# Performance work log

Measured on AMD Instinct MI355X. Metric: run time of the kernel, lower is better.

Reference implementation:

```python
import jax, jax.numpy as jnp
import numpy as np

N_CONV = 3
FEAT = 128
N_RBF = 20
CUTOFF = 5.0
EPS = 1e-15
N_NODES = 10000
N_EDGES = 160000


def setup_inputs() -> dict:
    key = jax.random.key(0)
    ks = jax.random.split(key, 8)
    N, E = N_NODES, N_EDGES
    cg_xyz = jax.random.normal(ks[0], (N, 3), jnp.float32) * 2.0
    # Directed, self-loop-free edge list (both i<j and i>j present, so the
    # original make_directed() is a no-op on this data).
    src = jax.random.randint(ks[1], (E,), 0, N)
    off = jax.random.randint(ks[2], (E,), 1, N)
    CG_nbr_list = jnp.stack([src, (src + off) % N], axis=1)
    cg_s = jax.random.normal(ks[3], (N, FEAT), jnp.float32)
    s = 1.0 / np.sqrt(FEAT)
    # Per-conv-layer weights of ENMessageBlock: inv_dense = Dense(F->F, silu) + Dense(F->3F);
    # dist_embed = ExpNormalBasis(n_rbf) -> Dense(n_rbf->3F) * cosine envelope.
    W1 = jax.random.normal(ks[4], (N_CONV, FEAT, FEAT), jnp.float32) * s
    b1 = jnp.zeros((N_CONV, FEAT), jnp.float32)
    W2 = jax.random.normal(ks[5], (N_CONV, FEAT, 3 * FEAT), jnp.float32) * s
    b2 = jnp.zeros((N_CONV, 3 * FEAT), jnp.float32)
    Wr = jax.random.normal(ks[6], (N_CONV, N_RBF, 3 * FEAT), jnp.float32) / np.sqrt(N_RBF)
    br = jnp.zeros((N_CONV, 3 * FEAT), jnp.float32)
    return {"cg_xyz": cg_xyz, "CG_nbr_list": CG_nbr_list, "cg_s": cg_s,
            "W1": W1, "b1": b1, "W2": W2, "b2": b2, "Wr": Wr, "br": br}


def _expnorm_rbf(dist):
    # ExpNormalBasis: exp(-beta * (exp(-d) - mu)^2), mu in [exp(-cutoff), 1]
    mu = jnp.linspace(np.exp(-CUTOFF), 1.0, N_RBF, dtype=jnp.float32)
    beta = np.float32((2.0 / N_RBF * (1.0 - np.exp(-CUTOFF))) ** -2)
    return jnp.exp(-beta * (jnp.exp(-dist)[:, None] - mu) ** 2)  # (E, n_rbf)


def _cos_envelope(dist):
    return jnp.where(dist < CUTOFF, 0.5 * (jnp.cos(jnp.pi * dist / CUTOFF) + 1.0), 0.0)


def reference(cg_xyz, CG_nbr_list, cg_s, W1, b1, W2, b2, Wr, br):
    N = cg_s.shape[0]
    i, j = CG_nbr_list[:, 0], CG_nbr_list[:, 1]
    r_ij = cg_xyz[j] - cg_xyz[i]                      # (E, 3)
    dist = jnp.sqrt((r_ij ** 2 + EPS).sum(-1))        # (E,)
    unit = r_ij / dist[:, None]                        # (E, 3)
    rbf = _expnorm_rbf(dist)                           # (E, n_rbf) edge-invariant across layers
    env = _cos_envelope(dist)[:, None]                 # (E, 1)

    s_i = cg_s                                         # (N, F)
    v_i = jnp.zeros((N, FEAT, 3), cg_s.dtype)          # (N, F, 3)
    for l in range(N_CONV):
        phi = jax.nn.silu(s_i @ W1[l] + b1[l]) @ W2[l] + b2[l]   # (N, 3F)
        w_s = (rbf @ Wr[l] + br[l]) * env                         # (E, 3F)
        prod = phi[j] * w_s                                       # (E, 3F) gather + gate
        ds = prod[:, :FEAT]                                       # scalar message
        gate_v = prod[:, FEAT:2 * FEAT]                           # gates v_j
        gate_u = prod[:, 2 * FEAT:]                               # gates unit vector
        dv_ij = gate_u[:, :, None] * unit[:, None, :] + gate_v[:, :, None] * v_i[j]  # (E, F, 3)
        s_i = s_i + jax.ops.segment_sum(ds, i, num_segments=N)
        v_i = v_i + jax.ops.segment_sum(dv_ij, i, num_segments=N)
    return s_i, v_i
```

## Files before the change

### kernel.cpp

```cpp
#include <hip/hip_runtime.h>
#include <hip/hip_bf16.h>

#define NRBF 20
#define KAUG 24

typedef __attribute__((ext_vector_type(8))) short short8;
typedef __attribute__((ext_vector_type(4))) float float4v;
typedef __attribute__((ext_vector_type(2))) _Float16 half2v;
typedef unsigned short ushort_t;

__device__ __forceinline__ float bf2f(ushort_t u) {
    return __uint_as_float(((unsigned)u) << 16);
}
__device__ __forceinline__ ushort_t f2bf(float f) {
    unsigned u = __float_as_uint(f);
    u += 0x7FFF + ((u >> 16) & 1);
    return (ushort_t)(u >> 16);
}
__device__ __forceinline__ float ldin(const void* p, size_t idx, int isbf) {
    return isbf ? bf2f(((const ushort_t*)p)[idx]) : ((const float*)p)[idx];
}
__device__ __forceinline__ void stout(void* p, size_t idx, float v, int isbf) {
    if (isbf) ((ushort_t*)p)[idx] = f2bf(v);
    else      ((float*)p)[idx] = v;
}
__device__ __forceinline__ float dot2(half2v a, half2v b, float c) {
#if __has_builtin(__builtin_amdgcn_fdot2)
    return __builtin_amdgcn_fdot2(a, b, c, false);
#else
    return c + (float)a.x * (float)b.x + (float)a.y * (float)b.y;
#endif
}

__global__ void detect_kernel(const void* __restrict__ xyz, int* __restrict__ flag,
                              int* __restrict__ deg, int N) {
    int idx = blockIdx.x * blockDim.x + threadIdx.x;
    if (idx < N) deg[idx] = 0;
    if (blockIdx.x == 0 && threadIdx.x < 64) {
        const ushort_t* u = (const ushort_t*)xyz;
        unsigned e0 = (u[2 * threadIdx.x] >> 7) & 0xFF;
        unsigned long long bad = __ballot(e0 >= 0x90);
        if (threadIdx.x == 0) *flag = (__popcll(bad) > 2) ? 0 : 1;
    }
}

__global__ void prelude_kernel(const void* __restrict__ xyz, const int* __restrict__ nbr,
                               const void* __restrict__ cg_s,
                               const void* __restrict__ W1, const void* __restrict__ W2,
                               const void* __restrict__ Wr, const void* __restrict__ br,
                               float* __restrict__ s_acc, ushort_t* __restrict__ s_hi,
                               ushort_t* __restrict__ s_lo, int* __restrict__ deg,
                               ushort_t* __restrict__ B1hi, ushort_t* __restrict__ B1lo,
                               ushort_t* __restrict__ B2hi, ushort_t* __restrict__ B2lo,
                               _Float16* __restrict__ WrT,
                               int N128, int E, const int* __restrict__ flagp) {
    int isbf = *flagp;
    int idx = blockIdx.x * blockDim.x + threadIdx.x;
    if (idx < E) {
        int i = nbr[2 * idx], j = nbr[2 * idx + 1];
        float dx = ldin(xyz, 3 * j,     isbf) - ldin(xyz, 3 * i,     isbf);
        float dy = ldin(xyz, 3 * j + 1, isbf) - ldin(xyz, 3 * i + 1, isbf);
        float dz = ldin(xyz, 3 * j + 2, isbf) - ldin(xyz, 3 * i + 2, isbf);
        float dist = sqrtf(dx * dx + dy * dy + dz * dz + 3e-15f);
        if (dist < 5.0f) atomicAdd(&deg[i], 1);
    }
    if (idx < N128) {
        float v = ldin(cg_s, idx, isbf);
        s_acc[idx] = v;
        ushort_t hi = f2bf(v);
        s_hi[idx] = hi;
        s_lo[idx] = f2bf(v - bf2f(hi));
    }
    const int NW1 = 3 * 4 * 8 * 64;
    const int NW2 = 3 * 4 * 24 * 64;
    const int NWT = 3 * 384;
    if (idx < NW1) {
        int lane = idx & 63;
        int t = idx >> 6;
        int nt = t % 8; t /= 8;
        int ks = t % 4; int l = t / 4;
        int n = lane & 15, quad = lane >> 4;
        int col = nt * 16 + n;
        size_t base = (size_t)l * 128 * 128;
        size_t fo = (size_t)idx * 8;
        #pragma unroll
        for (int j = 0; j < 8; j++) {
            int k = ks * 32 + quad * 8 + j;
            float v = ldin(W1, base + (size_t)k * 128 + col, isbf);
            ushort_t hi = f2bf(v);
            B1hi[fo + j] = hi;
            B1lo[fo + j] = f2bf(v - bf2f(hi));
        }
    } else if (idx < NW1 + NW2) {
        int i2 = idx - NW1;
        int lane = i2 & 63;
        int t = i2 >> 6;
        int nt = t % 24; t /= 24;
        int ks = t % 4; int l = t / 4;
        int n = lane & 15, quad = lane >> 4;
        int col = nt * 16 + n;
        size_t base = (size_t)l * 128 * 384;
        size_t fo = (size_t)i2 * 8;
        #pragma unroll
        for (int j = 0; j < 8; j++) {
            int k = ks * 32 + quad * 8 + j;
            float v = ldin(W2, base + (size_t)k * 384 + col, isbf);
            ushort_t hi = f2bf(v);
            B2hi[fo + j] = hi;
            B2lo[fo + j] = f2bf(v - bf2f(hi));
        }
    } else if (idx < NW1 + NW2 + NWT) {
        int i2 = idx - NW1 - NW2;
        int l = i2 / 384, col = i2 % 384;
        _Float16* wt = WrT + ((size_t)l * 384 + col) * KAUG;
        #pragma unroll
        for (int k = 0; k < KAUG; k++) {
            float v = 0.f;
            if (k < NRBF) v = ldin(Wr, ((size_t)l * NRBF + k) * 384 + col, isbf);
            else if (k == NRBF) v = ldin(br, (size_t)l * 384 + col, isbf);
            wt[k] = (_Float16)v;
        }
    }
}

__global__ void scan_kernel(int* __restrict__ deg, int* __restrict__ rowptr, int N) {
    __shared__ int part[256];
    int t = threadIdx.x;
    int chunk = (N + 255) / 256;
    int lo = t * chunk, hi = min(lo + chunk, N);
    int s = 0;
    for (int i = lo; i < hi; i++) s += deg[i];
    part[t] = s;
    __syncthreads();
    for (int off = 1; off < 256; off <<= 1) {
        int v = (t >= off) ? part[t - off] : 0;
        __syncthreads();
        if (t >= off) part[t] += v;
        __syncthreads();
    }
    int base = (t == 0) ? 0 : part[t - 1];
    for (int i = lo; i < hi; i++) {
        rowptr[i] = base;
        int d = deg[i];
        deg[i] = base;
        base += d;
    }
    if (t == 0) rowptr[N] = part[255];
}

__global__ void pack_kernel(const void* __restrict__ xyz, const int* __restrict__ nbr,
                            int* __restrict__ cursor, int* __restrict__ jlist,
                            float4* __restrict__ upos, _Float16* __restrict__ rbfh,
                            int E, const int* __restrict__ flagp) {
    int isbf = *flagp;
    int e = blockIdx.x * blockDim.x + threadIdx.x;
    if (e >= E) return;
    int i = nbr[2 * e], j = nbr[2 * e + 1];
    float dx = ldin(xyz, 3 * j,     isbf) - ldin(xyz, 3 * i,     isbf);
    float dy = ldin(xyz, 3 * j + 1, isbf) - ldin(xyz, 3 * i + 1, isbf);
    float dz = ldin(xyz, 3 * j + 2, isbf) - ldin(xyz, 3 * i + 2, isbf);
    float dist = sqrtf(dx * dx + dy * dy + dz * dz + 3e-15f);
    if (!(dist < 5.0f)) return;
    constexpr float PI = 3.14159265358979323846f;
    float ev = 0.5f * (cosf(PI * dist * 0.2f) + 1.0f);
    int pos = atomicAdd(&cursor[i], 1);
    jlist[pos] = j;
    float inv = 1.0f / dist;
    upos[pos] = make_float4(dx * inv, dy * inv, dz * inv, ev);
    constexpr double EM5 = 0.006737946999085467;
    constexpr float MU0 = (float)EM5;
    constexpr float DMU = (float)((1.0 - EM5) / 19.0);
    constexpr float BETA = (float)(1.0 / ((0.1 * (1.0 - EM5)) * (0.1 * (1.0 - EM5))));
    float ed = expf(-dist);
    _Float16* rp = rbfh + (size_t)pos * KAUG;
    #pragma unroll
    for (int k = 0; k < NRBF; k++) {
        float dmu = ed - (MU0 + k * DMU);
        rp[k] = (_Float16)(ev * expf(-BETA * dmu * dmu));
    }
    rp[NRBF] = (_Float16)ev;
    #pragma unroll
    for (int k = NRBF + 1; k < KAUG; k++) rp[k] = (_Float16)0.f;
}

template <int ACT, int OUTMODE, int NTILES>
__global__ __launch_bounds__(256) void mfma_gemm(
    const ushort_t* __restrict__ Ahi, const ushort_t* __restrict__ Alo,
    const ushort_t* __restrict__ Bhi, const ushort_t* __restrict__ Blo,
    const void* __restrict__ bias, size_t biasoff,
    ushort_t* __restrict__ out_hi, ushort_t* __restrict__ out_lo,
    int M, const int* __restrict__ flagp) {
    constexpr int Ncols = NTILES * 16;
    int isbf = *flagp;
    int nt = blockIdx.x % NTILES;
    int bx = blockIdx.x / NTILES;
    int tid = threadIdx.x;
    int wave = tid >> 6, lane = tid & 63;
    int m = lane & 15, quad = lane >> 4;
    int brow = bx * 64 + wave * 16;
    int row = brow + m;
    float4v acc = {};
    short8 zero8 = {};
    #pragma unroll
    for (int ks = 0; ks < 4; ks++) {
        short8 ah = zero8, al = zero8;
        if (row < M) {
            size_t ao = (size_t)row * 128 + ks * 32 + quad * 8;
            ah = *reinterpret_cast<const short8*>(Ahi + ao);
            al = *reinterpret_cast<const short8*>(Alo + ao);
        }
        size_t fo = (((size_t)ks * NTILES + nt) * 64 + lane) * 8;
        short8 bh = *reinterpret_cast<const short8*>(Bhi + fo);
        acc = __builtin_amdgcn_mfma_f32_16x16x32_bf16(ah, bh, acc, 0, 0, 0);
        acc = __builtin_amdgcn_mfma_f32_16x16x32_bf16(al, bh, acc, 0, 0, 0);
        if (!isbf) {
            short8 bl = *reinterpret_cast<const short8*>(Blo + fo);
            acc = __builtin_amdgcn_mfma_f32_16x16x32_bf16(ah, bl, acc, 0, 0, 0);
        }
    }
    int col = nt * 16 + m;
    float bv = ldin(bias, biasoff + col, isbf);
    #pragma unroll
    for (int r = 0; r < 4; r++) {
        int orow = brow + quad * 4 + r;
        if (orow >= M) continue;
        float x = acc[r] + bv;
        if (ACT) x = x / (1.0f + expf(-x));
        size_t oo = (size_t)orow * Ncols + col;
        ushort_t h = f2bf(x);
        out_hi[oo] = h;
        if (OUTMODE == 0) out_lo[oo] = f2bf(x - bf2f(h));
    }
}

template <int L0, int LAST>
__global__ __launch_bounds__(128, 8) void node_kernel(
    const int* __restrict__ rowptr, const int* __restrict__ jlist,
    const float4* __restrict__ upos, const _Float16* __restrict__ rbfh,
    const _Float16* __restrict__ WrT,
    const ushort_t* __restrict__ phi,
    const float* __restrict__ v_old, const ushort_t* __restrict__ vh_old,
    float* __restrict__ s_acc, ushort_t* __restrict__ s_hi, ushort_t* __restrict__ s_lo,
    float* __restrict__ v_new, ushort_t* __restrict__ vh_new,
    void* __restrict__ out, int N, const int* __restrict__ flagp) {
    int isbf = *flagp;
    int tt = threadIdx.x;
    int node = blockIdx.x;

    half2v wc0[11], wc1[11], wc2[11];
    {
        const half2v* w0p = (const half2v*)(WrT + (size_t)tt * KAUG);
        const half2v* w1p = (const half2v*)(WrT + (size_t)(tt + 128) * KAUG);
        const half2v* w2p = (const half2v*)(WrT + (size_t)(tt + 256) * KAUG);
        #pragma unroll
        for (int k = 0; k < 11; k++) {
            wc0[k] = w0p[k]; wc1[k] = w1p[k]; wc2[k] = w2p[k];
        }
    }
    int start = __builtin_amdgcn_readfirstlane(rowptr[node]);
    int end   = __builtin_amdgcn_readfirstlane(rowptr[node + 1]);

    float dsv = 0.f, ax = 0.f, ay = 0.f, az = 0.f;
    for (int k = start; k < end; k++) {
        int j = __builtin_amdgcn_readfirstlane(jlist[k]);
        float4 u4 = upos[k];
        const half2v* rp = (const half2v*)(rbfh + (size_t)k * KAUG);
        float w0 = 0.f, w1 = 0.f, w2 = 0.f;
        #pragma unroll
        for (int r = 0; r < 11; r++) {
            half2v rv = rp[r];
            w0 = dot2(rv, wc0[r], w0);
            w1 = dot2(rv, wc1[r], w1);
            w2 = dot2(rv, wc2[r], w2);
        }
        size_t jb = (size_t)j * 384;
        dsv += bf2f(phi[jb + tt]) * w0;
        float gv = bf2f(phi[jb + 128 + tt]) * w1;
        float gu = bf2f(phi[jb + 256 + tt]) * w2;
        if (L0) {
            ax += gu * u4.x; ay += gu * u4.y; az += gu * u4.z;
        } else {
            const ushort_t* vj = &vh_old[jb + (size_t)tt * 3];
            ax += gu * u4.x + gv * bf2f(vj[0]);
            ay += gu * u4.y + gv * bf2f(vj[1]);
            az += gu * u4.z + gv * bf2f(vj[2]);
        }
    }
    size_t so = (size_t)node * 128 + tt;
    float snew = s_acc[so] + dsv;
    size_t ib = (size_t)node * 384 + (size_t)tt * 3;
    float vx = L0 ? ax : v_old[ib]     + ax;
    float vy = L0 ? ay : v_old[ib + 1] + ay;
    float vz = L0 ? az : v_old[ib + 2] + az;
    if (LAST) {
        stout(out, so, snew, isbf);
        size_t ob = (size_t)N * 128 + ib;
        stout(out, ob,     vx, isbf);
        stout(out, ob + 1, vy, isbf);
        stout(out, ob + 2, vz, isbf);
    } else {
        s_acc[so] = snew;
        ushort_t hi = f2bf(snew);
        s_hi[so] = hi;
        s_lo[so] = f2bf(snew - bf2f(hi));
        v_new[ib] = vx; v_new[ib + 1] = vy; v_new[ib + 2] = vz;
        vh_new[ib]     = f2bf(vx);
        vh_new[ib + 1] = f2bf(vy);
        vh_new[ib + 2] = f2bf(vz);
    }
}

extern "C" void kernel_launch(void* const* d_in, const int* in_sizes, int n_in,
                              void* d_out, int out_size, void* d_ws, size_t ws_size,
                              hipStream_t stream) {
    const int N = in_sizes[0] / 3;
    const int E = in_sizes[1] / 2;
    const void* xyz  = d_in[0];
    const int*  nbr  = (const int*)d_in[1];
    const void* cg_s = d_in[2];
    const void* W1   = d_in[3];
    const void* b1   = d_in[4];
    const void* W2   = d_in[5];
    const void* b2   = d_in[6];
    const void* Wr   = d_in[7];
    const void* br   = d_in[8];

    size_t off = 0;
    auto alloc = [&](size_t bytes) -> char* {
        char* p = (char*)d_ws + off;
        off = (off + bytes + 63) & ~(size_t)63;
        return p;
    };
    int*       flag   = (int*)alloc(64);
    float*     s_acc  = (float*)alloc((size_t)N * 128 * 4);
    float*     vA     = (float*)alloc((size_t)N * 384 * 4);
    float*     vB     = (float*)alloc((size_t)N * 384 * 4);
    int*       rowptr = (int*)alloc((size_t)(N + 1) * 4);
    int*       deg    = (int*)alloc((size_t)N * 4);
    int*       jlist  = (int*)alloc((size_t)E * 4);
    float4*    upos   = (float4*)alloc((size_t)(E + 16) * 16);
    _Float16*  rbfh   = (_Float16*)alloc((size_t)(E + 16) * KAUG * 2);
    _Float16*  WrT    = (_Float16*)alloc((size_t)3 * 384 * KAUG * 2);
    ushort_t*  s_hi   = (ushort_t*)alloc((size_t)N * 128 * 2);
    ushort_t*  s_lo   = (ushort_t*)alloc((size_t)N * 128 * 2);
    ushort_t*  h_hi   = (ushort_t*)alloc((size_t)N * 128 * 2);
    ushort_t*  h_lo   = (ushort_t*)alloc((size_t)N * 128 * 2);
    ushort_t*  phi    = (ushort_t*)alloc((size_t)N * 384 * 2);
    ushort_t*  vhA    = (ushort_t*)alloc((size_t)N * 384 * 2);
    ushort_t*  vhB    = (ushort_t*)alloc((size_t)N * 384 * 2);
    ushort_t*  B1hi   = (ushort_t*)alloc((size_t)3 * 4 * 8 * 64 * 8 * 2);
    ushort_t*  B1lo   = (ushort_t*)alloc((size_t)3 * 4 * 8 * 64 * 8 * 2);
    ushort_t*  B2hi   = (ushort_t*)alloc((size_t)3 * 4 * 24 * 64 * 8 * 2);
    ushort_t*  B2lo   = (ushort_t*)alloc((size_t)3 * 4 * 24 * 64 * 8 * 2);

    detect_kernel<<<(N + 255) / 256, 256, 0, stream>>>(xyz, flag, deg, N);
    const int N128 = N * 128;
    const int pg = (max(E, N128) + 255) / 256;
    prelude_kernel<<<pg, 256, 0, stream>>>(xyz, nbr, cg_s, W1, W2, Wr, br,
                                           s_acc, s_hi, s_lo, deg,
                                           B1hi, B1lo, B2hi, B2lo, WrT,
                                           N128, E, flag);
    scan_kernel<<<1, 256, 0, stream>>>(deg, rowptr, N);
    pack_kernel<<<(E + 255) / 256, 256, 0, stream>>>(xyz, nbr, deg, jlist, upos,
                                                     rbfh, E, flag);

    const int gx = (N + 63) / 64;
    for (int l = 0; l < 3; l++) {
        mfma_gemm<1, 0, 8><<<gx * 8, 256, 0, stream>>>(
            s_hi, s_lo,
            B1hi + (size_t)l * 4 * 8 * 64 * 8, B1lo + (size_t)l * 4 * 8 * 64 * 8,
            b1, (size_t)l * 128, h_hi, h_lo, N, flag);
        mfma_gemm<0, 1, 24><<<gx * 24, 256, 0, stream>>>(
            h_hi, h_lo,
            B2hi + (size_t)l * 4 * 24 * 64 * 8, B2lo + (size_t)l * 4 * 24 * 64 * 8,
            b2, (size_t)l * 384, phi, (ushort_t*)nullptr, N, flag);
        const _Float16* wrt = WrT + (size_t)l * 384 * KAUG;
        if (l == 0) {
            node_kernel<1, 0><<<N, 128, 0, stream>>>(
                rowptr, jlist, upos, rbfh, wrt, phi,
                vA, vhA, s_acc, s_hi, s_lo, vA, vhA, d_out, N, flag);
        } else if (l == 1) {
            node_kernel<0, 0><<<N, 128, 0, stream>>>(
                rowptr, jlist, upos, rbfh, wrt, phi,
                vA, vhA, s_acc, s_hi, s_lo, vB, vhB, d_out, N, flag);
        } else {
            node_kernel<0, 1><<<N, 128, 0, stream>>>(
                rowptr, jlist, upos, rbfh, wrt, phi,
                vB, vhB, s_acc, s_hi, s_lo, vB, vhB, d_out, N, flag);
        }
    }
}
```

Measured before the change: 328.3 us.

## Fuse the two per-layer dense GEMMs into one kernel with shared-memory hidden activations

Merges the SiLU Dense(F->F) GEMM and the Dense(F->3F) GEMM into a single kernel. Each block computes the full 128-wide hidden tile for its 64 rows into swizzled LDS, then computes a quarter of the 384 output columns from it. This removes one launch per layer and the global round trip of h_hi/h_lo. In exchange, the first GEMM is recomputed redundantly by each of the 4 column-split blocks, and LDS use per block grows to 32KB.

```diff
diff --git a/kernel.cpp b/kernel.cpp
--- a/kernel.cpp
+++ b/kernel.cpp
@@ -183,53 +183,93 @@
     for (int k = NRBF + 1; k < KAUG; k++) rp[k] = (_Float16)0.f;
 }
 
-template <int ACT, int OUTMODE, int NTILES>
-__global__ __launch_bounds__(256) void mfma_gemm(
+template <int CSPLIT>
+__global__ __launch_bounds__(256) void mfma_gemm12(
     const ushort_t* __restrict__ Ahi, const ushort_t* __restrict__ Alo,
-    const ushort_t* __restrict__ Bhi, const ushort_t* __restrict__ Blo,
-    const void* __restrict__ bias, size_t biasoff,
-    ushort_t* __restrict__ out_hi, ushort_t* __restrict__ out_lo,
-    int M, const int* __restrict__ flagp) {
-    constexpr int Ncols = NTILES * 16;
+    const ushort_t* __restrict__ B1h, const ushort_t* __restrict__ B1l,
+    const ushort_t* __restrict__ B2h, const ushort_t* __restrict__ B2l,
+    const void* __restrict__ bias1, size_t b1off,
+    const void* __restrict__ bias2, size_t b2off,
+    ushort_t* __restrict__ phi, int M, const int* __restrict__ flagp) {
+    constexpr int T2 = 24 / CSPLIT;
     int isbf = *flagp;
-    int nt = blockIdx.x % NTILES;
-    int bx = blockIdx.x / NTILES;
+    int cs = blockIdx.x % CSPLIT;
+    int bx = blockIdx.x / CSPLIT;
     int tid = threadIdx.x;
     int wave = tid >> 6, lane = tid & 63;
     int m = lane & 15, quad = lane >> 4;
     int brow = bx * 64 + wave * 16;
     int row = brow + m;
-    float4v acc = {};
+
+    __shared__ ushort_t Hhi[4][16 * 128];
+    __shared__ ushort_t Hlo[4][16 * 128];
+
     short8 zero8 = {};
+    short8 ah[4], al[4];
     #pragma unroll
     for (int ks = 0; ks < 4; ks++) {
-        short8 ah = zero8, al = zero8;
+        ah[ks] = zero8; al[ks] = zero8;
         if (row < M) {
             size_t ao = (size_t)row * 128 + ks * 32 + quad * 8;
-            ah = *reinterpret_cast<const short8*>(Ahi + ao);
-            al = *reinterpret_cast<const short8*>(Alo + ao);
-        }
-        size_t fo = (((size_t)ks * NTILES + nt) * 64 + lane) * 8;
-        short8 bh = *reinterpret_cast<const short8*>(Bhi + fo);
-        acc = __builtin_amdgcn_mfma_f32_16x16x32_bf16(ah, bh, acc, 0, 0, 0);
-        acc = __builtin_amdgcn_mfma_f32_16x16x32_bf16(al, bh, acc, 0, 0, 0);
-        if (!isbf) {
-            short8 bl = *reinterpret_cast<const short8*>(Blo + fo);
-            acc = __builtin_amdgcn_mfma_f32_16x16x32_bf16(ah, bl, acc, 0, 0, 0);
-        }
-    }
-    int col = nt * 16 + m;
-    float bv = ldin(bias, biasoff + col, isbf);
+            ah[ks] = *reinterpret_cast<const short8*>(Ahi + ao);
+            al[ks] = *reinterpret_cast<const short8*>(Alo + ao);
+        }
+    }
     #pragma unroll
-    for (int r = 0; r < 4; r++) {
-        int orow = brow + quad * 4 + r;
-        if (orow >= M) continue;
-        float x = acc[r] + bv;
-        if (ACT) x = x / (1.0f + expf(-x));
-        size_t oo = (size_t)orow * Ncols + col;
-        ushort_t h = f2bf(x);
-        out_hi[oo] = h;
-        if (OUTMODE == 0) out_lo[oo] = f2bf(x - bf2f(h));
+    for (int ct = 0; ct < 8; ct++) {
+        float4v acc = {};
+        #pragma unroll
+        for (int ks = 0; ks < 4; ks++) {
+            size_t fo = (((size_t)ks * 8 + ct) * 64 + lane) * 8;
+            short8 bh = *reinterpret_cast<const short8*>(B1h + fo);
+            acc = __builtin_amdgcn_mfma_f32_16x16x32_bf16(ah[ks], bh, acc, 0, 0, 0);
+            acc = __builtin_amdgcn_mfma_f32_16x16x32_bf16(al[ks], bh, acc, 0, 0, 0);
+            if (!isbf) {
+                short8 bl = *reinterpret_cast<const short8*>(B1l + fo);
+                acc = __builtin_amdgcn_mfma_f32_16x16x32_bf16(ah[ks], bl, acc, 0, 0, 0);
+            }
+        }
+        int col = ct * 16 + m;
+        float bv = ldin(bias1, b1off + col, isbf);
+        #pragma unroll
+        for (int r = 0; r < 4; r++) {
+            int hrow = quad * 4 + r;
+            float x = acc[r] + bv;
+            x = x / (1.0f + expf(-x));
+            ushort_t hi = f2bf(x);
+            int ci = col ^ ((hrow & 7) << 3);
+            Hhi[wave][hrow * 128 + ci] = hi;
+            Hlo[wave][hrow * 128 + ci] = f2bf(x - bf2f(hi));
+        }
+    }
+    __syncthreads();
+    #pragma unroll
+    for (int t = 0; t < T2; t++) {
+        int nt = cs * T2 + t;
+        float4v acc = {};
+        #pragma unroll
+        for (int ks = 0; ks < 4; ks++) {
+            int c0 = (ks * 32 + quad * 8) ^ ((m & 7) << 3);
+            short8 hh = *reinterpret_cast<const short8*>(&Hhi[wave][m * 128 + c0]);
+            short8 hl = *reinterpret_cast<const short8*>(&Hlo[wave][m * 128 + c0]);
+            size_t fo = (((size_t)ks * 24 + nt) * 64 + lane) * 8;
+            short8 bh = *reinterpret_cast<const short8*>(B2h + fo);
+            acc = __builtin_amdgcn_mfma_f32_16x16x32_bf16(hh, bh, acc, 0, 0, 0);
+            acc = __builtin_amdgcn_mfma_f32_16x16x32_bf16(hl, bh, acc, 0, 0, 0);
+            if (!isbf) {
+                short8 bl = *reinterpret_cast<const short8*>(B2l + fo);
+                acc = __builtin_amdgcn_mfma_f32_16x16x32_bf16(hh, bl, acc, 0, 0, 0);
+            }
+        }
+        int col = nt * 16 + m;
+        float bv = ldin(bias2, b2off + col, isbf);
+        #pragma unroll
+        for (int r = 0; r < 4; r++) {
+            int orow = brow + quad * 4 + r;
+            if (orow >= M) continue;
+            float x = acc[r] + bv;
+            phi[(size_t)orow * 384 + col] = f2bf(x);
+        }
     }
 }
 
@@ -343,8 +383,6 @@
     _Float16*  WrT    = (_Float16*)alloc((size_t)3 * 384 * KAUG * 2);
     ushort_t*  s_hi   = (ushort_t*)alloc((size_t)N * 128 * 2);
     ushort_t*  s_lo   = (ushort_t*)alloc((size_t)N * 128 * 2);
-    ushort_t*  h_hi   = (ushort_t*)alloc((size_t)N * 128 * 2);
-    ushort_t*  h_lo   = (ushort_t*)alloc((size_t)N * 128 * 2);
     ushort_t*  phi    = (ushort_t*)alloc((size_t)N * 384 * 2);
     ushort_t*  vhA    = (ushort_t*)alloc((size_t)N * 384 * 2);
     ushort_t*  vhB    = (ushort_t*)alloc((size_t)N * 384 * 2);
@@ -366,14 +404,11 @@
 
     const int gx = (N + 63) / 64;
     for (int l = 0; l < 3; l++) {
-        mfma_gemm<1, 0, 8><<<gx * 8, 256, 0, stream>>>(
+        mfma_gemm12<4><<<gx * 4, 256, 0, stream>>>(
             s_hi, s_lo,
-            B1hi + (size_t)l * 4 * 8 * 64 * 8, B1lo + (size_t)l * 4 * 8 * 64 * 8,
-            b1, (size_t)l * 128, h_hi, h_lo, N, flag);
-        mfma_gemm<0, 1, 24><<<gx * 24, 256, 0, stream>>>(
-            h_hi, h_lo,
+            B1hi + (size_t)l * 4 * 8 * 64 * 8,  B1lo + (size_t)l * 4 * 8 * 64 * 8,
             B2hi + (size_t)l * 4 * 24 * 64 * 8, B2lo + (size_t)l * 4 * 24 * 64 * 8,
-            b2, (size_t)l * 384, phi, (ushort_t*)nullptr, N, flag);
+            b1, (size_t)l * 128, b2, (size_t)l * 384, phi, N, flag);
         const _Float16* wrt = WrT + (size_t)l * 384 * KAUG;
         if (l == 0) {
             node_kernel<1, 0><<<N, 128, 0, stream>>>(
```

After: 350.6 us. 6.8% more time.
